# Performance work log

Hardware: AMD Instinct MI355X
Metric: run time of the kernel (lower is better)

The kernel has to match this reference:

```python
import jax, jax.numpy as jnp
import numpy as np

N, D, M, E = 8192, 2048, 512, 4
SCALE = 1.0

def setup_inputs() -> dict:
    key = jax.random.key(0)
    ks = jax.random.split(key, 6)
    x = jax.random.normal(ks[0], (N, D), dtype=jnp.float32)
    domains = jax.random.randint(ks[1], (N,), 0, E, dtype=jnp.int64)
    # torch Linear default init ~ U(-1/sqrt(fan_in), 1/sqrt(fan_in)); use scaled normals
    W1 = jax.random.normal(ks[2], (E, M, D), dtype=jnp.float32) / np.sqrt(D)
    b1 = jax.random.normal(ks[3], (E, M), dtype=jnp.float32) * 0.01
    W2 = jax.random.normal(ks[4], (E, D, M), dtype=jnp.float32) / np.sqrt(M)
    b2 = jax.random.normal(ks[5], (E, D), dtype=jnp.float32) * 0.01
    return {"x": x, "domains": domains, "W1": W1, "b1": b1, "W2": W2, "b2": b2}

def reference(x, domains, W1, b1, W2, b2):
    # Each expert: Linear(D->M) -> ReLU -> Linear(M->D); token n uses expert domains[n].
    # Dense compute over all experts, then per-token select via one-hot (jit-friendly
    # equivalent of the boolean-mask gather/scatter in the torch code).
    h = jax.nn.relu(jnp.einsum('nd,emd->enm', x, W1) + b1[:, None, :])   # [E,N,M]
    y = jnp.einsum('enm,edm->end', h, W2) + b2[:, None, :]               # [E,N,D]
    sel = jax.nn.one_hot(domains, E, dtype=x.dtype)                       # [N,E]
    out = x + SCALE * jnp.einsum('end,ne->nd', y, sel)
    return out
```

## Files before the change

### kernel.cpp

```cpp
#include <hip/hip_runtime.h>
#include <hip/hip_bf16.h>
#include <cstdint>
#include <type_traits>

#define N_TOK 8192
#define DDIM  2048
#define MDIM  512
#define NEXP  4
#define PADROWS (N_TOK + NEXP * 256)

typedef __bf16 bf16x4 __attribute__((ext_vector_type(4)));
typedef __bf16 bf16x8 __attribute__((ext_vector_type(8)));
typedef float  f32x4  __attribute__((ext_vector_type(4)));

__device__ int g_counts[NEXP];
__device__ int g_idx[NEXP * N_TOK];
__device__ __align__(16) __hip_bfloat16 g_Xp[(size_t)(DDIM / 64) * PADROWS * 64];
__device__ __align__(16) __hip_bfloat16 g_Hp[(size_t)(MDIM / 64) * PADROWS * 64];
__device__ __align__(16) __hip_bfloat16 g_W1t[(size_t)NEXP * MDIM * DDIM];
__device__ __align__(16) __hip_bfloat16 g_W2t[(size_t)NEXP * DDIM * MDIM];

__global__ void zero_counts_kernel() {
    if (threadIdx.x < NEXP) g_counts[threadIdx.x] = 0;
}

__global__ void bucket_kernel(const void* __restrict__ domv) {
    const int i    = blockIdx.x * blockDim.x + threadIdx.x;
    const int lane = threadIdx.x & 63;

    const long long* d64 = (const long long*)domv;
    long long probe = d64[lane];
    bool mode64 = (__ballot(probe >= 0 && probe < NEXP) == ~0ull);

    const int e = mode64 ? (int)d64[i] : ((const int*)domv)[i];

#pragma unroll
    for (int ex = 0; ex < NEXP; ++ex) {
        unsigned long long m = __ballot(e == ex);
        if (m == 0) continue;
        int cnt    = __popcll(m);
        int leader = __ffsll((long long)m) - 1;
        int base   = 0;
        if (lane == leader) base = atomicAdd(&g_counts[ex], cnt);
        base = __shfl(base, leader);
        if (e == ex) {
            int prefix = __popcll(m & ((1ull << lane) - 1ull));
            g_idx[ex * N_TOK + base + prefix] = i;
        }
    }
}

__global__ __launch_bounds__(256)
void cvt_w_kernel(const float* __restrict__ w1, const float* __restrict__ w2) {
    const bool is1 = (blockIdx.y == 0);
    const float* src = is1 ? w1 : w2;
    __hip_bfloat16* dst = is1 ? g_W1t : g_W2t;
    const int total8 = NEXP * MDIM * DDIM / 8;
    const int stride = gridDim.x * blockDim.x;
    for (int g8 = blockIdx.x * blockDim.x + threadIdx.x; g8 < total8; g8 += stride) {
        const int e   = g8 >> 17;
        const int rem = g8 & 131071;
        int row, kt, within;
        if (is1) { row = rem >> 8; int d0 = (rem & 255) * 8; kt = d0 >> 6; within = d0 & 63; }
        else     { row = rem >> 6; int m0 = (rem & 63) * 8;  kt = m0 >> 6; within = m0 & 63; }
        const float* s = src + (size_t)g8 * 8;
        f32x4 a = *(const f32x4*)s;
        f32x4 b = *(const f32x4*)(s + 4);
        bf16x8 r;
        r[0] = (__bf16)a[0]; r[1] = (__bf16)a[1]; r[2] = (__bf16)a[2]; r[3] = (__bf16)a[3];
        r[4] = (__bf16)b[0]; r[5] = (__bf16)b[1]; r[6] = (__bf16)b[2]; r[7] = (__bf16)b[3];
        const size_t d = is1 ? (((size_t)(e * 32 + kt) * MDIM + row) * 64 + within)
                             : (((size_t)(e * 8 + kt) * DDIM + row) * 64 + within);
        *(bf16x8*)&dst[d] = r;
    }
}

__global__ __launch_bounds__(256)
void cvt_xp_kernel(const float* __restrict__ x) {
    int c[NEXP], off[NEXP + 1]; off[0] = 0;
#pragma unroll
    for (int e = 0; e < NEXP; ++e) { c[e] = g_counts[e]; off[e + 1] = off[e] + ((c[e] + 255) & ~255); }

    const int gs = blockIdx.x;
    int e = 0;
#pragma unroll
    for (int t = 0; t < NEXP - 1; ++t) if (gs >= off[t + 1]) e = t + 1;
    if (gs >= off[e + 1]) return;
    int ls = gs - off[e];
    if (ls >= c[e]) ls = c[e] - 1;
    const int tok = g_idx[e * N_TOK + ls];

    const int d0 = threadIdx.x * 8;
    const float* s = x + (size_t)tok * DDIM + d0;
    f32x4 a = *(const f32x4*)s;
    f32x4 b = *(const f32x4*)(s + 4);
    bf16x8 r;
    r[0] = (__bf16)a[0]; r[1] = (__bf16)a[1]; r[2] = (__bf16)a[2]; r[3] = (__bf16)a[3];
    r[4] = (__bf16)b[0]; r[5] = (__bf16)b[1]; r[6] = (__bf16)b[2]; r[7] = (__bf16)b[3];
    *(bf16x8*)&g_Xp[((size_t)(d0 >> 6) * PADROWS + gs) * 64 + (d0 & 63)] = r;
}

__device__ __forceinline__ void gl16(const __hip_bfloat16* g, __hip_bfloat16* l) {
    __builtin_amdgcn_global_load_lds(
        (const __attribute__((address_space(1))) void*)g,
        (__attribute__((address_space(3))) void*)l,
        16, 0, 0);
}

template <int N>
__device__ __forceinline__ void wait_vm() {
    if constexpr (N == 0)      asm volatile("s_waitcnt vmcnt(0)" ::: "memory");
    else if constexpr (N == 6) asm volatile("s_waitcnt vmcnt(6)" ::: "memory");
    else if constexpr (N == 8) asm volatile("s_waitcnt vmcnt(8)" ::: "memory");
    else                       asm volatile("s_waitcnt vmcnt(0)" ::: "memory");
}

template <int BN, int KDIM, int NCOLS, bool RELU, bool TILEOUT, typename TC>
__device__ __forceinline__ void gemm_core(const __hip_bfloat16* __restrict__ A,
                                          const __hip_bfloat16* __restrict__ B,
                                          const float* __restrict__ bias,
                                          const float* __restrict__ resid,
                                          TC* __restrict__ C) {
    constexpr int BM    = 128;
    constexpr int BK    = 64;
    constexpr int KTS   = KDIM / BK;
    constexpr int NACH  = 4;
    constexpr int NBCH  = BN / 32;
    constexpr int LPS   = NACH + NBCH;
    constexpr int NJ    = BN / 32;
    constexpr int NSTEP = KTS;

    const int rt = blockIdx.x;
    const int ct = blockIdx.y;

    int cv[NEXP], off[NEXP + 1]; off[0] = 0;
#pragma unroll
    for (int x = 0; x < NEXP; ++x) { cv[x] = g_counts[x]; off[x + 1] = off[x] + ((cv[x] + 255) & ~255); }
    const int r0 = rt * BM;
    if (r0 >= off[NEXP]) return;
    int e = 0;
#pragma unroll
    for (int t = 0; t < NEXP - 1; ++t) if (r0 >= off[t + 1]) e = t + 1;

    __shared__ __align__(16) __hip_bfloat16 sA[2][BM * BK];
    __shared__ __align__(16) __hip_bfloat16 sB[2][BN * BK];
    __shared__ int sTok[BM];

    const int tid  = threadIdx.x;
    const int wave = tid >> 6;
    const int lane = tid & 63;

    if (!TILEOUT) {
        if (tid < BM) {
            int ls = r0 + tid - off[e];
            sTok[tid] = (ls < cv[e]) ? g_idx[e * N_TOK + ls] : -1;
        }
        __syncthreads();
    }

    const int srow = wave * 8 + (lane >> 3);
    const int ssl  = ((lane & 7) ^ (lane >> 3)) * 8;

    auto stage = [&](int buf, int kt) {
#pragma unroll
        for (int q = 0; q < NACH; ++q)
            gl16(A + ((size_t)kt * PADROWS + r0 + q * 32 + srow) * 64 + ssl,
                 &sA[buf][(q * 256 + wave * 64) * 8]);
#pragma unroll
        for (int q = 0; q < NBCH; ++q)
            gl16(B + ((size_t)(e * KTS + kt) * NCOLS + ct * BN + q * 32 + srow) * 64 + ssl,
                 &sB[buf][(q * 256 + wave * 64) * 8]);
    };

    const int wm   = (wave >> 1) * 64;
    const int wn   = (wave & 1) * (BN / 2);
    const int frow = lane & 15;
    int cof[2];
#pragma unroll
    for (int ks = 0; ks < 2; ++ks)
        cof[ks] = ((ks * 4 + (lane >> 4)) ^ (lane & 7)) * 8;

    f32x4 acc[4][NJ] = {};

    auto compute = [&](int buf) {
        const __hip_bfloat16* pA = &sA[buf][0];
        const __hip_bfloat16* pB = &sB[buf][0];
#pragma unroll
        for (int ks = 0; ks < 2; ++ks) {
            bf16x8 bfr[NJ];
#pragma unroll
            for (int j = 0; j < NJ; ++j)
                bfr[j] = *(const bf16x8*)&pB[(wn + j * 16 + frow) * BK + cof[ks]];
#pragma unroll
            for (int i = 0; i < 4; ++i) {
                bf16x8 af = *(const bf16x8*)&pA[(wm + i * 16 + frow) * BK + cof[ks]];
#pragma unroll
                for (int j = 0; j < NJ; ++j)
                    acc[i][j] = __builtin_amdgcn_mfma_f32_16x16x32_bf16(
                        bfr[j], af, acc[i][j], 0, 0, 0);
            }
        }
    };

    stage(0, 0);
    stage(1, 1);

    int cur = 0;
    for (int t = 0; t < NSTEP - 1; ++t) {
        wait_vm<LPS>();
        __builtin_amdgcn_s_barrier();
        __builtin_amdgcn_sched_barrier(0);
        compute(cur);
        asm volatile("" ::: "memory");
        __builtin_amdgcn_s_barrier();
        if (t + 2 < NSTEP) stage(cur, t + 2);
        cur ^= 1;
    }
    wait_vm<0>();
    __builtin_amdgcn_s_barrier();
    __builtin_amdgcn_sched_barrier(0);
    compute(cur);

    const int lrow = lane & 15;
    const int lcol = (lane >> 4) * 4;
#pragma unroll
    for (int i = 0; i < 4; ++i) {
        const int rl = wm + i * 16 + lrow;
        const int gs = r0 + rl;
#pragma unroll
        for (int j = 0; j < NJ; ++j) {
            const int col = ct * BN + wn + j * 16 + lcol;
            const f32x4 bv = *(const f32x4*)&bias[(size_t)e * NCOLS + col];
            f32x4 v = acc[i][j] + bv;
            if (RELU) {
#pragma unroll
                for (int r = 0; r < 4; ++r) v[r] = fmaxf(v[r], 0.0f);
            }
            if constexpr (TILEOUT) {
                bf16x4 h;
                h[0] = (__bf16)v[0]; h[1] = (__bf16)v[1];
                h[2] = (__bf16)v[2]; h[3] = (__bf16)v[3];
                *(bf16x4*)&C[((size_t)(col >> 6) * PADROWS + gs) * 64 + (col & 63)] = h;
            } else {
                const int tk = sTok[rl];
                if (tk >= 0) {
                    v += *(const f32x4*)&resid[(size_t)tk * NCOLS + col];
                    *(f32x4*)&C[(size_t)tk * NCOLS + col] = v;
                }
            }
        }
    }
}

__global__ __launch_bounds__(256)
void gemm1_kernel(const float* __restrict__ b1) {
    gemm_core<64, DDIM, MDIM, true, true, __hip_bfloat16>(
        g_Xp, g_W1t, b1, nullptr, g_Hp);
}

__global__ __launch_bounds__(256)
void gemm2_kernel(const float* __restrict__ x,
                  const float* __restrict__ b2,
                  float* __restrict__ out) {
    gemm_core<128, MDIM, DDIM, false, false, float>(
        g_Hp, g_W2t, b2, x, out);
}

extern "C" void kernel_launch(void* const* d_in, const int* in_sizes, int n_in,
                              void* d_out, int out_size, void* d_ws, size_t ws_size,
                              hipStream_t stream) {
    const float* x  = (const float*)d_in[0];
    const void*  dm = d_in[1];
    const float* W1 = (const float*)d_in[2];
    const float* b1 = (const float*)d_in[3];
    const float* W2 = (const float*)d_in[4];
    const float* b2 = (const float*)d_in[5];
    float* out = (float*)d_out;

    zero_counts_kernel<<<1, 64, 0, stream>>>();
    bucket_kernel<<<N_TOK / 256, 256, 0, stream>>>(dm);
    cvt_w_kernel<<<dim3(1024, 2), 256, 0, stream>>>(W1, W2);
    cvt_xp_kernel<<<PADROWS, 256, 0, stream>>>(x);

    gemm1_kernel<<<dim3(PADROWS / 128, MDIM / 64), 256, 0, stream>>>(b1);
    gemm2_kernel<<<dim3(PADROWS / 128, DDIM / 128), 256, 0, stream>>>(x, b2, out);
}
```

Baseline: 241.8 us.

## Enlarge GEMM tiles, use BK=32 four-stage pipeline, XCD swizzle, merge conversion kernels

Both expert GEMMs move to larger tiles: 128x128 with 4 waves for the first and 256x256 with 8 waves for the second. The K-tile shrinks to 32 with a 4-deep LDS ring buffer and staged vmcnt waits. The packed bf16 activation and weight layouts change to 32-wide K chunks to match, with a new LDS swizzle. Blocks are remapped so neighbouring tiles land on the same XCD, and the X and weight conversion kernels are merged into one launch. The aim is more operand reuse per tile, deeper prefetch and fewer launches, at the cost of much more LDS per block and lower occupancy.

```diff
diff --git a/kernel.cpp b/kernel.cpp
--- a/kernel.cpp
+++ b/kernel.cpp
@@ -15,8 +15,8 @@
 
 __device__ int g_counts[NEXP];
 __device__ int g_idx[NEXP * N_TOK];
-__device__ __align__(16) __hip_bfloat16 g_Xp[(size_t)(DDIM / 64) * PADROWS * 64];
-__device__ __align__(16) __hip_bfloat16 g_Hp[(size_t)(MDIM / 64) * PADROWS * 64];
+__device__ __align__(16) __hip_bfloat16 g_Xp[(size_t)DDIM * PADROWS];
+__device__ __align__(16) __hip_bfloat16 g_Hp[(size_t)MDIM * PADROWS];
 __device__ __align__(16) __hip_bfloat16 g_W1t[(size_t)NEXP * MDIM * DDIM];
 __device__ __align__(16) __hip_bfloat16 g_W2t[(size_t)NEXP * DDIM * MDIM];
 
@@ -51,53 +51,55 @@
 }
 
 __global__ __launch_bounds__(256)
-void cvt_w_kernel(const float* __restrict__ w1, const float* __restrict__ w2) {
-    const bool is1 = (blockIdx.y == 0);
-    const float* src = is1 ? w1 : w2;
-    __hip_bfloat16* dst = is1 ? g_W1t : g_W2t;
-    const int total8 = NEXP * MDIM * DDIM / 8;
-    const int stride = gridDim.x * blockDim.x;
-    for (int g8 = blockIdx.x * blockDim.x + threadIdx.x; g8 < total8; g8 += stride) {
+void cvt_all_kernel(const float* __restrict__ x,
+                    const float* __restrict__ w1,
+                    const float* __restrict__ w2) {
+    if (blockIdx.y == 0) {
+        int c[NEXP], off[NEXP + 1]; off[0] = 0;
+#pragma unroll
+        for (int e = 0; e < NEXP; ++e) { c[e] = g_counts[e]; off[e + 1] = off[e] + ((c[e] + 255) & ~255); }
+        const int gs = blockIdx.x;
+        int e = 0;
+#pragma unroll
+        for (int t = 0; t < NEXP - 1; ++t) if (gs >= off[t + 1]) e = t + 1;
+        if (gs >= off[e + 1]) return;
+        int ls = gs - off[e];
+        if (ls >= c[e]) ls = c[e] - 1;
+        if (ls < 0) ls = 0;
+        const int tok = g_idx[e * N_TOK + ls];
+
+        const int d0 = threadIdx.x * 8;
+        const float* s = x + (size_t)tok * DDIM + d0;
+        f32x4 a = *(const f32x4*)s;
+        f32x4 b = *(const f32x4*)(s + 4);
+        bf16x8 r;
+        r[0] = (__bf16)a[0]; r[1] = (__bf16)a[1]; r[2] = (__bf16)a[2]; r[3] = (__bf16)a[3];
+        r[4] = (__bf16)b[0]; r[5] = (__bf16)b[1]; r[6] = (__bf16)b[2]; r[7] = (__bf16)b[3];
+        *(bf16x8*)&g_Xp[((size_t)(d0 >> 5) * PADROWS + gs) * 32 + (d0 & 31)] = r;
+    } else {
+        constexpr int HALF = NEXP * MDIM * DDIM / 8;
+        const int gtid = blockIdx.x * 256 + threadIdx.x;
+        if (gtid >= 2 * HALF) return;
+        const bool is1 = (gtid < HALF);
+        const int g8 = is1 ? gtid : gtid - HALF;
+        const float* src = is1 ? w1 : w2;
+        __hip_bfloat16* dst = is1 ? g_W1t : g_W2t;
+
         const int e   = g8 >> 17;
         const int rem = g8 & 131071;
         int row, kt, within;
-        if (is1) { row = rem >> 8; int d0 = (rem & 255) * 8; kt = d0 >> 6; within = d0 & 63; }
-        else     { row = rem >> 6; int m0 = (rem & 63) * 8;  kt = m0 >> 6; within = m0 & 63; }
+        if (is1) { row = rem >> 8; int d0 = (rem & 255) * 8; kt = d0 >> 5; within = d0 & 31; }
+        else     { row = rem >> 6; int m0 = (rem & 63) * 8;  kt = m0 >> 5; within = m0 & 31; }
         const float* s = src + (size_t)g8 * 8;
         f32x4 a = *(const f32x4*)s;
         f32x4 b = *(const f32x4*)(s + 4);
         bf16x8 r;
         r[0] = (__bf16)a[0]; r[1] = (__bf16)a[1]; r[2] = (__bf16)a[2]; r[3] = (__bf16)a[3];
         r[4] = (__bf16)b[0]; r[5] = (__bf16)b[1]; r[6] = (__bf16)b[2]; r[7] = (__bf16)b[3];
-        const size_t d = is1 ? (((size_t)(e * 32 + kt) * MDIM + row) * 64 + within)
-                             : (((size_t)(e * 8 + kt) * DDIM + row) * 64 + within);
+        const size_t d = is1 ? (((size_t)(e * 64 + kt) * MDIM + row) * 32 + within)
+                             : (((size_t)(e * 16 + kt) * DDIM + row) * 32 + within);
         *(bf16x8*)&dst[d] = r;
     }
-}
-
-__global__ __launch_bounds__(256)
-void cvt_xp_kernel(const float* __restrict__ x) {
-    int c[NEXP], off[NEXP + 1]; off[0] = 0;
-#pragma unroll
-    for (int e = 0; e < NEXP; ++e) { c[e] = g_counts[e]; off[e + 1] = off[e] + ((c[e] + 255) & ~255); }
-
-    const int gs = blockIdx.x;
-    int e = 0;
-#pragma unroll
-    for (int t = 0; t < NEXP - 1; ++t) if (gs >= off[t + 1]) e = t + 1;
-    if (gs >= off[e + 1]) return;
-    int ls = gs - off[e];
-    if (ls >= c[e]) ls = c[e] - 1;
-    const int tok = g_idx[e * N_TOK + ls];
-
-    const int d0 = threadIdx.x * 8;
-    const float* s = x + (size_t)tok * DDIM + d0;
-    f32x4 a = *(const f32x4*)s;
-    f32x4 b = *(const f32x4*)(s + 4);
-    bf16x8 r;
-    r[0] = (__bf16)a[0]; r[1] = (__bf16)a[1]; r[2] = (__bf16)a[2]; r[3] = (__bf16)a[3];
-    r[4] = (__bf16)b[0]; r[5] = (__bf16)b[1]; r[6] = (__bf16)b[2]; r[7] = (__bf16)b[3];
-    *(bf16x8*)&g_Xp[((size_t)(d0 >> 6) * PADROWS + gs) * 64 + (d0 & 63)] = r;
 }
 
 __device__ __forceinline__ void gl16(const __hip_bfloat16* g, __hip_bfloat16* l) {
@@ -109,29 +111,37 @@
 
 template <int N>
 __device__ __forceinline__ void wait_vm() {
-    if constexpr (N == 0)      asm volatile("s_waitcnt vmcnt(0)" ::: "memory");
-    else if constexpr (N == 6) asm volatile("s_waitcnt vmcnt(6)" ::: "memory");
-    else if constexpr (N == 8) asm volatile("s_waitcnt vmcnt(8)" ::: "memory");
-    else                       asm volatile("s_waitcnt vmcnt(0)" ::: "memory");
-}
-
-template <int BN, int KDIM, int NCOLS, bool RELU, bool TILEOUT, typename TC>
+    if constexpr (N == 0)       asm volatile("s_waitcnt vmcnt(0)" ::: "memory");
+    else if constexpr (N == 4)  asm volatile("s_waitcnt vmcnt(4)" ::: "memory");
+    else if constexpr (N == 8)  asm volatile("s_waitcnt vmcnt(8)" ::: "memory");
+    else if constexpr (N == 12) asm volatile("s_waitcnt vmcnt(12)" ::: "memory");
+}
+
+template <int BM, int BN, int NWAVE, int WVN, int KDIM, int NCOLS,
+          bool RELU, bool TILEOUT, typename TC>
 __device__ __forceinline__ void gemm_core(const __hip_bfloat16* __restrict__ A,
                                           const __hip_bfloat16* __restrict__ B,
                                           const float* __restrict__ bias,
                                           const float* __restrict__ resid,
                                           TC* __restrict__ C) {
-    constexpr int BM    = 128;
-    constexpr int BK    = 64;
-    constexpr int KTS   = KDIM / BK;
-    constexpr int NACH  = 4;
-    constexpr int NBCH  = BN / 32;
-    constexpr int LPS   = NACH + NBCH;
-    constexpr int NJ    = BN / 32;
-    constexpr int NSTEP = KTS;
-
-    const int rt = blockIdx.x;
-    const int ct = blockIdx.y;
+    constexpr int BK      = 32;
+    constexpr int KT      = KDIM / BK;
+    constexpr int THREADS = NWAVE * 64;
+    constexpr int RPP     = THREADS / 4;
+    constexpr int APASS   = BM / RPP;
+    constexpr int BPASS   = BN / RPP;
+    constexpr int WM      = BM / (NWAVE / WVN);
+    constexpr int WN      = BN / WVN;
+    constexpr int NI      = WM / 16;
+    constexpr int NJ      = WN / 16;
+    constexpr int NRT     = PADROWS / BM;
+    constexpr int NWG     = NRT * (NCOLS / BN);
+    static_assert(NWG % 8 == 0, "bijective XCD swizzle needs nwg%8==0");
+
+    const int bid = blockIdx.x;
+    const int swz = (bid & 7) * (NWG / 8) + (bid >> 3);
+    const int rt  = swz % NRT;
+    const int ct  = swz / NRT;
 
     int cv[NEXP], off[NEXP + 1]; off[0] = 0;
 #pragma unroll
@@ -142,8 +152,8 @@
 #pragma unroll
     for (int t = 0; t < NEXP - 1; ++t) if (r0 >= off[t + 1]) e = t + 1;
 
-    __shared__ __align__(16) __hip_bfloat16 sA[2][BM * BK];
-    __shared__ __align__(16) __hip_bfloat16 sB[2][BN * BK];
+    __shared__ __align__(16) __hip_bfloat16 sA[4][BM * BK];
+    __shared__ __align__(16) __hip_bfloat16 sB[4][BN * BK];
     __shared__ int sTok[BM];
 
     const int tid  = threadIdx.x;
@@ -155,76 +165,66 @@
             int ls = r0 + tid - off[e];
             sTok[tid] = (ls < cv[e]) ? g_idx[e * N_TOK + ls] : -1;
         }
-        __syncthreads();
-    }
-
-    const int srow = wave * 8 + (lane >> 3);
-    const int ssl  = ((lane & 7) ^ (lane >> 3)) * 8;
+    }
+
+    const int srow = wave * 16 + (lane >> 2);
+    const int ssl  = ((lane & 3) ^ ((lane >> 3) & 3)) * 8;
 
     auto stage = [&](int buf, int kt) {
 #pragma unroll
-        for (int q = 0; q < NACH; ++q)
-            gl16(A + ((size_t)kt * PADROWS + r0 + q * 32 + srow) * 64 + ssl,
-                 &sA[buf][(q * 256 + wave * 64) * 8]);
-#pragma unroll
-        for (int q = 0; q < NBCH; ++q)
-            gl16(B + ((size_t)(e * KTS + kt) * NCOLS + ct * BN + q * 32 + srow) * 64 + ssl,
-                 &sB[buf][(q * 256 + wave * 64) * 8]);
+        for (int p = 0; p < APASS; ++p)
+            gl16(A + ((size_t)kt * PADROWS + r0 + p * RPP + srow) * BK + ssl,
+                 &sA[buf][(p * RPP + wave * 16) * BK]);
+#pragma unroll
+        for (int p = 0; p < BPASS; ++p)
+            gl16(B + ((size_t)(e * KT + kt) * NCOLS + ct * BN + p * RPP + srow) * BK + ssl,
+                 &sB[buf][(p * RPP + wave * 16) * BK]);
     };
 
-    const int wm   = (wave >> 1) * 64;
-    const int wn   = (wave & 1) * (BN / 2);
+    const int wm   = (wave / WVN) * WM;
+    const int wn   = (wave % WVN) * WN;
     const int frow = lane & 15;
-    int cof[2];
-#pragma unroll
-    for (int ks = 0; ks < 2; ++ks)
-        cof[ks] = ((ks * 4 + (lane >> 4)) ^ (lane & 7)) * 8;
-
-    f32x4 acc[4][NJ] = {};
+    const int cof  = (((lane >> 4) ^ ((lane >> 1) & 3))) * 8;
+
+    f32x4 acc[NI][NJ] = {};
 
     auto compute = [&](int buf) {
         const __hip_bfloat16* pA = &sA[buf][0];
         const __hip_bfloat16* pB = &sB[buf][0];
-#pragma unroll
-        for (int ks = 0; ks < 2; ++ks) {
-            bf16x8 bfr[NJ];
+        bf16x8 bfr[NJ];
+#pragma unroll
+        for (int j = 0; j < NJ; ++j)
+            bfr[j] = *(const bf16x8*)&pB[(wn + j * 16 + frow) * BK + cof];
+#pragma unroll
+        for (int i = 0; i < NI; ++i) {
+            bf16x8 af = *(const bf16x8*)&pA[(wm + i * 16 + frow) * BK + cof];
 #pragma unroll
             for (int j = 0; j < NJ; ++j)
-                bfr[j] = *(const bf16x8*)&pB[(wn + j * 16 + frow) * BK + cof[ks]];
-#pragma unroll
-            for (int i = 0; i < 4; ++i) {
-                bf16x8 af = *(const bf16x8*)&pA[(wm + i * 16 + frow) * BK + cof[ks]];
-#pragma unroll
-                for (int j = 0; j < NJ; ++j)
-                    acc[i][j] = __builtin_amdgcn_mfma_f32_16x16x32_bf16(
-                        bfr[j], af, acc[i][j], 0, 0, 0);
-            }
+                acc[i][j] = __builtin_amdgcn_mfma_f32_16x16x32_bf16(
+                    bfr[j], af, acc[i][j], 0, 0, 0);
         }
     };
 
-    stage(0, 0);
-    stage(1, 1);
-
-    int cur = 0;
-    for (int t = 0; t < NSTEP - 1; ++t) {
-        wait_vm<LPS>();
+    stage(0, 0); stage(1, 1); stage(2, 2); stage(3, 3);
+
+    for (int t = 0; t < KT; ++t) {
+        const int rem = KT - 1 - t;
+        if (rem >= 3)      wait_vm<12>();
+        else if (rem == 2) wait_vm<8>();
+        else if (rem == 1) wait_vm<4>();
+        else               wait_vm<0>();
         __builtin_amdgcn_s_barrier();
         __builtin_amdgcn_sched_barrier(0);
-        compute(cur);
+        compute(t & 3);
         asm volatile("" ::: "memory");
         __builtin_amdgcn_s_barrier();
-        if (t + 2 < NSTEP) stage(cur, t + 2);
-        cur ^= 1;
-    }
-    wait_vm<0>();
-    __builtin_amdgcn_s_barrier();
-    __builtin_amdgcn_sched_barrier(0);
-    compute(cur);
+        if (t + 4 < KT) stage(t & 3, t + 4);
+    }
 
     const int lrow = lane & 15;
     const int lcol = (lane >> 4) * 4;
 #pragma unroll
-    for (int i = 0; i < 4; ++i) {
+    for (int i = 0; i < NI; ++i) {
         const int rl = wm + i * 16 + lrow;
         const int gs = r0 + rl;
 #pragma unroll
@@ -240,7 +240,7 @@
                 bf16x4 h;
                 h[0] = (__bf16)v[0]; h[1] = (__bf16)v[1];
                 h[2] = (__bf16)v[2]; h[3] = (__bf16)v[3];
-                *(bf16x4*)&C[((size_t)(col >> 6) * PADROWS + gs) * 64 + (col & 63)] = h;
+                *(bf16x4*)&C[((size_t)(col >> 5) * PADROWS + gs) * 32 + (col & 31)] = h;
             } else {
                 const int tk = sTok[rl];
                 if (tk >= 0) {
@@ -252,17 +252,17 @@
     }
 }
 
-__global__ __launch_bounds__(256)
+__global__ __launch_bounds__(256, 2)
 void gemm1_kernel(const float* __restrict__ b1) {
-    gemm_core<64, DDIM, MDIM, true, true, __hip_bfloat16>(
+    gemm_core<128, 128, 4, 2, DDIM, MDIM, true, true, __hip_bfloat16>(
         g_Xp, g_W1t, b1, nullptr, g_Hp);
 }
 
-__global__ __launch_bounds__(256)
+__global__ __launch_bounds__(512, 2)
 void gemm2_kernel(const float* __restrict__ x,
                   const float* __restrict__ b2,
                   float* __restrict__ out) {
-    gemm_core<128, MDIM, DDIM, false, false, float>(
+    gemm_core<256, 256, 8, 4, MDIM, DDIM, false, false, float>(
         g_Hp, g_W2t, b2, x, out);
 }
 
@@ -279,9 +279,8 @@
 
     zero_counts_kernel<<<1, 64, 0, stream>>>();
     bucket_kernel<<<N_TOK / 256, 256, 0, stream>>>(dm);
-    cvt_w_kernel<<<dim3(1024, 2), 256, 0, stream>>>(W1, W2);
-    cvt_xp_kernel<<<PADROWS, 256, 0, stream>>>(x);
-
-    gemm1_kernel<<<dim3(PADROWS / 128, MDIM / 64), 256, 0, stream>>>(b1);
-    gemm2_kernel<<<dim3(PADROWS / 128, DDIM / 128), 256, 0, stream>>>(x, b2, out);
-}
+    cvt_all_kernel<<<dim3(PADROWS, 2), 256, 0, stream>>>(x, W1, W2);
+
+    gemm1_kernel<<<72 * 4, 256, 0, stream>>>(b1);
+    gemm2_kernel<<<36 * 8, 512, 0, stream>>>(x, b2, out);
+}
```

Result: slower. 273.5 us (+13.1%).

## Fuse all stages into one persistent kernel with grid-wide barriers

Applied to the files above, without the earlier changes.

Replaces the six separate launches (zero counts, bucketing, weight conversion, token gather/convert, two GEMMs) with a single persistent kernel of 512 blocks that synchronises through a global atomic barrier. Bucketing becomes deterministic: per-block counts are followed by a block-level prefix scan, with no atomics on the token index. GEMM1 tile width goes from 64 to 128, and both GEMMs use a strided tile-to-block swizzle. This removes launch overhead and inter-kernel gaps, at the cost of relying on all 512 blocks being co-resident (deadlock risk otherwise), grid barrier latency, and fewer GEMM1 tiles for parallelism.

```diff
diff --git a/kernel.cpp b/kernel.cpp
--- a/kernel.cpp
+++ b/kernel.cpp
@@ -8,96 +8,39 @@
 #define MDIM  512
 #define NEXP  4
 #define PADROWS (N_TOK + NEXP * 256)
+#define NB   512
+#define NTHR 256
 
 typedef __bf16 bf16x4 __attribute__((ext_vector_type(4)));
 typedef __bf16 bf16x8 __attribute__((ext_vector_type(8)));
 typedef float  f32x4  __attribute__((ext_vector_type(4)));
 
+__device__ unsigned g_arrive;
+__device__ int g_blkcnt[NB][NEXP];
 __device__ int g_counts[NEXP];
 __device__ int g_idx[NEXP * N_TOK];
-__device__ __align__(16) __hip_bfloat16 g_Xp[(size_t)(DDIM / 64) * PADROWS * 64];
-__device__ __align__(16) __hip_bfloat16 g_Hp[(size_t)(MDIM / 64) * PADROWS * 64];
+__device__ __align__(16) __hip_bfloat16 g_Xp[(size_t)DDIM * PADROWS];
+__device__ __align__(16) __hip_bfloat16 g_Hp[(size_t)MDIM * PADROWS];
 __device__ __align__(16) __hip_bfloat16 g_W1t[(size_t)NEXP * MDIM * DDIM];
 __device__ __align__(16) __hip_bfloat16 g_W2t[(size_t)NEXP * DDIM * MDIM];
 
-__global__ void zero_counts_kernel() {
-    if (threadIdx.x < NEXP) g_counts[threadIdx.x] = 0;
-}
-
-__global__ void bucket_kernel(const void* __restrict__ domv) {
-    const int i    = blockIdx.x * blockDim.x + threadIdx.x;
-    const int lane = threadIdx.x & 63;
-
-    const long long* d64 = (const long long*)domv;
-    long long probe = d64[lane];
-    bool mode64 = (__ballot(probe >= 0 && probe < NEXP) == ~0ull);
-
-    const int e = mode64 ? (int)d64[i] : ((const int*)domv)[i];
-
-#pragma unroll
-    for (int ex = 0; ex < NEXP; ++ex) {
-        unsigned long long m = __ballot(e == ex);
-        if (m == 0) continue;
-        int cnt    = __popcll(m);
-        int leader = __ffsll((long long)m) - 1;
-        int base   = 0;
-        if (lane == leader) base = atomicAdd(&g_counts[ex], cnt);
-        base = __shfl(base, leader);
-        if (e == ex) {
-            int prefix = __popcll(m & ((1ull << lane) - 1ull));
-            g_idx[ex * N_TOK + base + prefix] = i;
-        }
-    }
-}
-
-__global__ __launch_bounds__(256)
-void cvt_w_kernel(const float* __restrict__ w1, const float* __restrict__ w2) {
-    const bool is1 = (blockIdx.y == 0);
-    const float* src = is1 ? w1 : w2;
-    __hip_bfloat16* dst = is1 ? g_W1t : g_W2t;
-    const int total8 = NEXP * MDIM * DDIM / 8;
-    const int stride = gridDim.x * blockDim.x;
-    for (int g8 = blockIdx.x * blockDim.x + threadIdx.x; g8 < total8; g8 += stride) {
-        const int e   = g8 >> 17;
-        const int rem = g8 & 131071;
-        int row, kt, within;
-        if (is1) { row = rem >> 8; int d0 = (rem & 255) * 8; kt = d0 >> 6; within = d0 & 63; }
-        else     { row = rem >> 6; int m0 = (rem & 63) * 8;  kt = m0 >> 6; within = m0 & 63; }
-        const float* s = src + (size_t)g8 * 8;
-        f32x4 a = *(const f32x4*)s;
-        f32x4 b = *(const f32x4*)(s + 4);
-        bf16x8 r;
-        r[0] = (__bf16)a[0]; r[1] = (__bf16)a[1]; r[2] = (__bf16)a[2]; r[3] = (__bf16)a[3];
-        r[4] = (__bf16)b[0]; r[5] = (__bf16)b[1]; r[6] = (__bf16)b[2]; r[7] = (__bf16)b[3];
-        const size_t d = is1 ? (((size_t)(e * 32 + kt) * MDIM + row) * 64 + within)
-                             : (((size_t)(e * 8 + kt) * DDIM + row) * 64 + within);
-        *(bf16x8*)&dst[d] = r;
-    }
-}
-
-__global__ __launch_bounds__(256)
-void cvt_xp_kernel(const float* __restrict__ x) {
-    int c[NEXP], off[NEXP + 1]; off[0] = 0;
-#pragma unroll
-    for (int e = 0; e < NEXP; ++e) { c[e] = g_counts[e]; off[e + 1] = off[e] + ((c[e] + 255) & ~255); }
-
-    const int gs = blockIdx.x;
-    int e = 0;
-#pragma unroll
-    for (int t = 0; t < NEXP - 1; ++t) if (gs >= off[t + 1]) e = t + 1;
-    if (gs >= off[e + 1]) return;
-    int ls = gs - off[e];
-    if (ls >= c[e]) ls = c[e] - 1;
-    const int tok = g_idx[e * N_TOK + ls];
-
-    const int d0 = threadIdx.x * 8;
-    const float* s = x + (size_t)tok * DDIM + d0;
-    f32x4 a = *(const f32x4*)s;
-    f32x4 b = *(const f32x4*)(s + 4);
-    bf16x8 r;
-    r[0] = (__bf16)a[0]; r[1] = (__bf16)a[1]; r[2] = (__bf16)a[2]; r[3] = (__bf16)a[3];
-    r[4] = (__bf16)b[0]; r[5] = (__bf16)b[1]; r[6] = (__bf16)b[2]; r[7] = (__bf16)b[3];
-    *(bf16x8*)&g_Xp[((size_t)(d0 >> 6) * PADROWS + gs) * 64 + (d0 & 63)] = r;
+struct SMem {
+    __hip_bfloat16 sA[2][128 * 64];
+    __hip_bfloat16 sB[2][128 * 64];
+    int sTok[128];
+};
+
+__device__ __forceinline__ void gsync() {
+    __syncthreads();
+    if (threadIdx.x == 0) {
+        __threadfence();
+        unsigned t = atomicAdd(&g_arrive, 1u);
+        unsigned target = (t & ~(unsigned)(NB - 1)) + NB;
+        while ((int)(atomicAdd(&g_arrive, 0u) - target) < 0)
+            __builtin_amdgcn_s_sleep(10);
+        __threadfence();
+    }
+    __syncthreads();
 }
 
 __device__ __forceinline__ void gl16(const __hip_bfloat16* g, __hip_bfloat16* l) {
@@ -110,50 +53,40 @@
 template <int N>
 __device__ __forceinline__ void wait_vm() {
     if constexpr (N == 0)      asm volatile("s_waitcnt vmcnt(0)" ::: "memory");
-    else if constexpr (N == 6) asm volatile("s_waitcnt vmcnt(6)" ::: "memory");
     else if constexpr (N == 8) asm volatile("s_waitcnt vmcnt(8)" ::: "memory");
-    else                       asm volatile("s_waitcnt vmcnt(0)" ::: "memory");
-}
-
-template <int BN, int KDIM, int NCOLS, bool RELU, bool TILEOUT, typename TC>
-__device__ __forceinline__ void gemm_core(const __hip_bfloat16* __restrict__ A,
-                                          const __hip_bfloat16* __restrict__ B,
-                                          const float* __restrict__ bias,
-                                          const float* __restrict__ resid,
-                                          TC* __restrict__ C) {
-    constexpr int BM    = 128;
-    constexpr int BK    = 64;
-    constexpr int KTS   = KDIM / BK;
-    constexpr int NACH  = 4;
-    constexpr int NBCH  = BN / 32;
-    constexpr int LPS   = NACH + NBCH;
-    constexpr int NJ    = BN / 32;
-    constexpr int NSTEP = KTS;
-
-    const int rt = blockIdx.x;
-    const int ct = blockIdx.y;
+}
+
+template <int KDIM, int NCOLS, bool RELU, bool TILEOUT, typename TC>
+__device__ void gemm_task(SMem* sm, int rt, int ct,
+                          const __hip_bfloat16* __restrict__ A,
+                          const __hip_bfloat16* __restrict__ B,
+                          const float* __restrict__ bias,
+                          const float* __restrict__ resid,
+                          TC* __restrict__ C) {
+    constexpr int BM  = 128;
+    constexpr int BN  = 128;
+    constexpr int BK  = 64;
+    constexpr int KT  = KDIM / BK;
+    constexpr int NJ  = 4;
 
     int cv[NEXP], off[NEXP + 1]; off[0] = 0;
 #pragma unroll
-    for (int x = 0; x < NEXP; ++x) { cv[x] = g_counts[x]; off[x + 1] = off[x] + ((cv[x] + 255) & ~255); }
+    for (int q = 0; q < NEXP; ++q) { cv[q] = g_counts[q]; off[q + 1] = off[q] + ((cv[q] + 255) & ~255); }
     const int r0 = rt * BM;
     if (r0 >= off[NEXP]) return;
     int e = 0;
 #pragma unroll
-    for (int t = 0; t < NEXP - 1; ++t) if (r0 >= off[t + 1]) e = t + 1;
-
-    __shared__ __align__(16) __hip_bfloat16 sA[2][BM * BK];
-    __shared__ __align__(16) __hip_bfloat16 sB[2][BN * BK];
-    __shared__ int sTok[BM];
+    for (int q = 0; q < NEXP - 1; ++q) if (r0 >= off[q + 1]) e = q + 1;
 
     const int tid  = threadIdx.x;
     const int wave = tid >> 6;
     const int lane = tid & 63;
 
+    __syncthreads();
     if (!TILEOUT) {
         if (tid < BM) {
             int ls = r0 + tid - off[e];
-            sTok[tid] = (ls < cv[e]) ? g_idx[e * N_TOK + ls] : -1;
+            sm->sTok[tid] = (ls < cv[e]) ? g_idx[e * N_TOK + ls] : -1;
         }
         __syncthreads();
     }
@@ -163,17 +96,17 @@
 
     auto stage = [&](int buf, int kt) {
 #pragma unroll
-        for (int q = 0; q < NACH; ++q)
+        for (int q = 0; q < 4; ++q)
             gl16(A + ((size_t)kt * PADROWS + r0 + q * 32 + srow) * 64 + ssl,
-                 &sA[buf][(q * 256 + wave * 64) * 8]);
-#pragma unroll
-        for (int q = 0; q < NBCH; ++q)
-            gl16(B + ((size_t)(e * KTS + kt) * NCOLS + ct * BN + q * 32 + srow) * 64 + ssl,
-                 &sB[buf][(q * 256 + wave * 64) * 8]);
+                 &sm->sA[buf][(q * 256 + wave * 64) * 8]);
+#pragma unroll
+        for (int q = 0; q < 4; ++q)
+            gl16(B + ((size_t)(e * KT + kt) * NCOLS + ct * BN + q * 32 + srow) * 64 + ssl,
+                 &sm->sB[buf][(q * 256 + wave * 64) * 8]);
     };
 
     const int wm   = (wave >> 1) * 64;
-    const int wn   = (wave & 1) * (BN / 2);
+    const int wn   = (wave & 1) * 64;
     const int frow = lane & 15;
     int cof[2];
 #pragma unroll
@@ -183,8 +116,8 @@
     f32x4 acc[4][NJ] = {};
 
     auto compute = [&](int buf) {
-        const __hip_bfloat16* pA = &sA[buf][0];
-        const __hip_bfloat16* pB = &sB[buf][0];
+        const __hip_bfloat16* pA = &sm->sA[buf][0];
+        const __hip_bfloat16* pB = &sm->sB[buf][0];
 #pragma unroll
         for (int ks = 0; ks < 2; ++ks) {
             bf16x8 bfr[NJ];
@@ -206,14 +139,14 @@
     stage(1, 1);
 
     int cur = 0;
-    for (int t = 0; t < NSTEP - 1; ++t) {
-        wait_vm<LPS>();
+    for (int t = 0; t < KT - 1; ++t) {
+        wait_vm<8>();
         __builtin_amdgcn_s_barrier();
         __builtin_amdgcn_sched_barrier(0);
         compute(cur);
         asm volatile("" ::: "memory");
         __builtin_amdgcn_s_barrier();
-        if (t + 2 < NSTEP) stage(cur, t + 2);
+        if (t + 2 < KT) stage(cur, t + 2);
         cur ^= 1;
     }
     wait_vm<0>();
@@ -242,7 +175,7 @@
                 h[2] = (__bf16)v[2]; h[3] = (__bf16)v[3];
                 *(bf16x4*)&C[((size_t)(col >> 6) * PADROWS + gs) * 64 + (col & 63)] = h;
             } else {
-                const int tk = sTok[rl];
+                const int tk = sm->sTok[rl];
                 if (tk >= 0) {
                     v += *(const f32x4*)&resid[(size_t)tk * NCOLS + col];
                     *(f32x4*)&C[(size_t)tk * NCOLS + col] = v;
@@ -252,18 +185,139 @@
     }
 }
 
-__global__ __launch_bounds__(256)
-void gemm1_kernel(const float* __restrict__ b1) {
-    gemm_core<64, DDIM, MDIM, true, true, __hip_bfloat16>(
-        g_Xp, g_W1t, b1, nullptr, g_Hp);
-}
-
-__global__ __launch_bounds__(256)
-void gemm2_kernel(const float* __restrict__ x,
-                  const float* __restrict__ b2,
+__global__ __launch_bounds__(NTHR, 2)
+void fused_kernel(const float* __restrict__ x, const void* __restrict__ dom,
+                  const float* __restrict__ w1, const float* __restrict__ b1,
+                  const float* __restrict__ w2, const float* __restrict__ b2,
                   float* __restrict__ out) {
-    gemm_core<128, MDIM, DDIM, false, false, float>(
-        g_Hp, g_W2t, b2, x, out);
+    __shared__ SMem sm;
+    const int bid  = blockIdx.x;
+    const int tid  = threadIdx.x;
+    const int lane = tid & 63;
+
+    {
+        constexpr int HALF = NEXP * MDIM * DDIM / 8;
+        for (int g = bid * NTHR + tid; g < 2 * HALF; g += NB * NTHR) {
+            const bool is1 = (g < HALF);
+            const int g8 = is1 ? g : g - HALF;
+            const float* src = is1 ? w1 : w2;
+            __hip_bfloat16* dst = is1 ? g_W1t : g_W2t;
+            const int e   = g8 >> 17;
+            const int rem = g8 & 131071;
+            int row, kt, within;
+            if (is1) { row = rem >> 8; int d0 = (rem & 255) * 8; kt = d0 >> 6; within = d0 & 63; }
+            else     { row = rem >> 6; int m0 = (rem & 63) * 8;  kt = m0 >> 6; within = m0 & 63; }
+            const float* s = src + (size_t)g8 * 8;
+            f32x4 a = *(const f32x4*)s;
+            f32x4 b = *(const f32x4*)(s + 4);
+            bf16x8 r;
+            r[0] = (__bf16)a[0]; r[1] = (__bf16)a[1]; r[2] = (__bf16)a[2]; r[3] = (__bf16)a[3];
+            r[4] = (__bf16)b[0]; r[5] = (__bf16)b[1]; r[6] = (__bf16)b[2]; r[7] = (__bf16)b[3];
+            const size_t d = is1 ? (((size_t)(e * 32 + kt) * MDIM + row) * 64 + within)
+                                 : (((size_t)(e * 8 + kt) * DDIM + row) * 64 + within);
+            *(bf16x8*)&dst[d] = r;
+        }
+    }
+    if (tid < 64) {
+        const long long* d64 = (const long long*)dom;
+        long long probe = d64[lane];
+        bool mode64 = (__ballot(probe >= 0 && probe < NEXP) == ~0ull);
+        int e = -1;
+        if (lane < 16) {
+            int i = bid * 16 + lane;
+            e = mode64 ? (int)d64[i] : ((const int*)dom)[i];
+        }
+#pragma unroll
+        for (int ex = 0; ex < NEXP; ++ex) {
+            unsigned long long m = __ballot(e == ex);
+            if (lane == 0) g_blkcnt[bid][ex] = __popcll(m);
+        }
+    }
+    gsync();
+
+    {
+        int (*sc)[256] = reinterpret_cast<int(*)[256]>(&sm.sA[0][0]);
+#pragma unroll
+        for (int e2 = 0; e2 < NEXP; ++e2)
+            sc[e2][tid] = g_blkcnt[2 * tid][e2] + g_blkcnt[2 * tid + 1][e2];
+        __syncthreads();
+        for (int o = 1; o < 256; o <<= 1) {
+            int v[NEXP];
+            if (tid >= o) {
+#pragma unroll
+                for (int e2 = 0; e2 < NEXP; ++e2) v[e2] = sc[e2][tid - o];
+            }
+            __syncthreads();
+            if (tid >= o) {
+#pragma unroll
+                for (int e2 = 0; e2 < NEXP; ++e2) sc[e2][tid] += v[e2];
+            }
+            __syncthreads();
+        }
+        if (tid < 64) {
+            const long long* d64 = (const long long*)dom;
+            long long probe = d64[lane];
+            bool mode64 = (__ballot(probe >= 0 && probe < NEXP) == ~0ull);
+            int e = -1;
+            if (lane < 16) {
+                int i = bid * 16 + lane;
+                e = mode64 ? (int)d64[i] : ((const int*)dom)[i];
+            }
+            const int q = bid >> 1;
+#pragma unroll
+            for (int ex = 0; ex < NEXP; ++ex) {
+                unsigned long long m = __ballot(e == ex);
+                if (e == ex) {
+                    int base = (q > 0 ? sc[ex][q - 1] : 0)
+                             + ((bid & 1) ? g_blkcnt[bid - 1][ex] : 0);
+                    int pos = base + __popcll(m & ((1ull << lane) - 1ull));
+                    g_idx[ex * N_TOK + pos] = bid * 16 + lane;
+                }
+            }
+        }
+        if (bid == 0 && tid < NEXP) g_counts[tid] = sc[tid][255];
+    }
+    gsync();
+
+    {
+        int cv[NEXP], off[NEXP + 1]; off[0] = 0;
+#pragma unroll
+        for (int e2 = 0; e2 < NEXP; ++e2) { cv[e2] = g_counts[e2]; off[e2 + 1] = off[e2] + ((cv[e2] + 255) & ~255); }
+        for (int ri = 0; ri < PADROWS / NB; ++ri) {
+            const int gs = bid * (PADROWS / NB) + ri;
+            int e = 0;
+#pragma unroll
+            for (int q = 0; q < NEXP - 1; ++q) if (gs >= off[q + 1]) e = q + 1;
+            if (gs < off[e + 1]) {
+                int ls = gs - off[e];
+                if (ls >= cv[e]) ls = cv[e] - 1;
+                if (ls < 0) ls = 0;
+                const int tok = g_idx[e * N_TOK + ls];
+                const int d0 = tid * 8;
+                const float* s = x + (size_t)tok * DDIM + d0;
+                f32x4 a = *(const f32x4*)s;
+                f32x4 b = *(const f32x4*)(s + 4);
+                bf16x8 r;
+                r[0] = (__bf16)a[0]; r[1] = (__bf16)a[1]; r[2] = (__bf16)a[2]; r[3] = (__bf16)a[3];
+                r[4] = (__bf16)b[0]; r[5] = (__bf16)b[1]; r[6] = (__bf16)b[2]; r[7] = (__bf16)b[3];
+                *(bf16x8*)&g_Xp[((size_t)(d0 >> 6) * PADROWS + gs) * 64 + (d0 & 63)] = r;
+            }
+        }
+    }
+    gsync();
+
+    for (int t = bid; t < 288; t += NB) {
+        const int s = (t & 7) * 36 + (t >> 3);
+        gemm_task<DDIM, MDIM, true, true, __hip_bfloat16>(
+            &sm, s % 72, s / 72, g_Xp, g_W1t, b1, nullptr, g_Hp);
+    }
+    gsync();
+
+    for (int t = bid; t < 1152; t += NB) {
+        const int s = (t & 7) * 144 + (t >> 3);
+        gemm_task<MDIM, DDIM, false, false, float>(
+            &sm, s % 72, s / 72, g_Hp, g_W2t, b2, x, out);
+    }
 }
 
 extern "C" void kernel_launch(void* const* d_in, const int* in_sizes, int n_in,
@@ -277,11 +331,5 @@
     const float* b2 = (const float*)d_in[5];
     float* out = (float*)d_out;
 
-    zero_counts_kernel<<<1, 64, 0, stream>>>();
-    bucket_kernel<<<N_TOK / 256, 256, 0, stream>>>(dm);
-    cvt_w_kernel<<<dim3(1024, 2), 256, 0, stream>>>(W1, W2);
-    cvt_xp_kernel<<<PADROWS, 256, 0, stream>>>(x);
-
-    gemm1_kernel<<<dim3(PADROWS / 128, MDIM / 64), 256, 0, stream>>>(b1);
-    gemm2_kernel<<<dim3(PADROWS / 128, DDIM / 128), 256, 0, stream>>>(x, b2, out);
-}
+    fused_kernel<<<NB, NTHR, 0, stream>>>(x, dm, W1, b1, W2, b2, out);
+}
```

New measurement: 430.3 us. 77.9% more time.
